# Performance work log

Measured on AMD Instinct MI355X. Metric: run time of the kernel, lower is better.

Reference implementation:

```python
import jax, jax.numpy as jnp
import numpy as np

L, N, C = 128, 32, 128
DIM_MLP, OUT = 128, 128


def setup_inputs() -> dict:
    key = jax.random.key(0)
    ks = jax.random.split(key, 6)
    s_in2 = 1.0 / np.sqrt(2 * C)
    s_mid = 1.0 / np.sqrt(DIM_MLP)
    s_in = 1.0 / np.sqrt(C)
    return {
        "x": jax.random.normal(ks[0], (L, N, C), jnp.float32),
        "attn_w1": jax.random.normal(ks[1], (2 * C, DIM_MLP), jnp.float32) * s_in2,
        "attn_b1": jnp.zeros((DIM_MLP,), jnp.float32),
        "attn_w2": jax.random.normal(ks[2], (DIM_MLP, OUT), jnp.float32) * s_mid,
        "attn_b2": jnp.zeros((OUT,), jnp.float32),
        "value_w1": jax.random.normal(ks[3], (C, DIM_MLP), jnp.float32) * s_in,
        "value_b1": jnp.zeros((DIM_MLP,), jnp.float32),
        "value_w2": jax.random.normal(ks[4], (DIM_MLP, OUT), jnp.float32) * s_mid,
        "value_b2": jnp.zeros((OUT,), jnp.float32),
    }


def reference(x, attn_w1, attn_b1, attn_w2, attn_b2,
              value_w1, value_b1, value_w2, value_b2):
    l, n, c = x.shape
    # Outer concat: pair[i, j, b] = concat(x[i, b], x[j, b])  -> (l, l, N, 2C)
    xi = jnp.broadcast_to(x[:, None, :, :], (l, l, n, c))
    xj = jnp.broadcast_to(x[None, :, :, :], (l, l, n, c))
    pair = jnp.concatenate([xi, xj], axis=-1)
    # Pairwise attention MLP (ReLU hidden, linear output)
    h = jax.nn.relu(pair @ attn_w1 + attn_b1)          # (l, l, N, dim_mlp)
    attn = h @ attn_w2 + attn_b2                       # (l, l, N, out)
    # Value MLP
    hv = jax.nn.relu(x @ value_w1 + value_b1)          # (l, N, dim_mlp)
    value = hv @ value_w2 + value_b2                   # (l, N, out)
    # Elementwise weighted reduce over key axis j (NOT a matmul over channels)
    out = jnp.einsum('ijbc,jbc->ibc', attn, value)     # (l, N, out)
    return out
```

## Files before the change

kernel.cpp:

```cpp
#include <hip/hip_runtime.h>
#include <hip/hip_bf16.h>

#define L_DIM 128
#define N_DIM 32
#define C_DIM 128
#define K_DIM 128
#define OUT_DIM 128

typedef __attribute__((ext_vector_type(8))) short short8;
typedef __attribute__((ext_vector_type(4))) float float4v;
typedef __attribute__((ext_vector_type(2))) float float2v;

static __device__ __forceinline__ short bf16_bits(float f) {
    __bf16 h = (__bf16)f;
    return __builtin_bit_cast(short, h);
}

__global__ __launch_bounds__(256) void k_pre(
    const float* __restrict__ x,
    const float* __restrict__ attn_w1, const float* __restrict__ attn_b1,
    const float* __restrict__ attn_w2,
    const float* __restrict__ value_w1, const float* __restrict__ value_b1,
    const float* __restrict__ value_w2, const float* __restrict__ value_b2,
    float* __restrict__ P, float* __restrict__ Q, float* __restrict__ V,
    short* __restrict__ W2s)
{
    int bid = blockIdx.x;
    if (bid >= 1024) {
        int e = (bid - 1024) * 256 + threadIdx.x;
        int idx  = e & 7;
        int colr = (e >> 3) & 15;
        int quad = (e >> 7) & 3;
        int mi   = (e >> 9) & 3;
        int ct   = e >> 11;
        int k = quad * 8 + 32 * mi + idx;
        int c = ct * 16 + colr;
        W2s[e] = bf16_bits(attn_w2[k * OUT_DIM + c]);
        return;
    }

    __shared__ float xs[4][C_DIM];
    __shared__ float hvs[4][K_DIM];
    int tid = threadIdx.x;
    int r0  = bid * 4;

    {
        int f = tid * 2;
        int row = f >> 7, c = f & 127;
        *(float2v*)(&xs[row][c]) = *(const float2v*)(x + (r0 + row) * C_DIM + c);
    }
    __syncthreads();

    int ks   = tid & 127;
    int half = tid >> 7;

    float pacc[2] = {0,0}, qacc[2] = {0,0}, hacc[2] = {0,0};
    #pragma unroll 4
    for (int c = 0; c < C_DIM; ++c) {
        float wa = attn_w1[c * K_DIM + ks];
        float wb = attn_w1[(C_DIM + c) * K_DIM + ks];
        float wv = value_w1[c * K_DIM + ks];
        #pragma unroll
        for (int r = 0; r < 2; ++r) {
            float xr = xs[half * 2 + r][c];
            pacc[r] = fmaf(xr, wa, pacc[r]);
            qacc[r] = fmaf(xr, wb, qacc[r]);
            hacc[r] = fmaf(xr, wv, hacc[r]);
        }
    }
    float b1 = attn_b1[ks], vb1 = value_b1[ks];
    #pragma unroll
    for (int r = 0; r < 2; ++r) {
        int rr = r0 + half * 2 + r;
        int i = rr >> 5, b = rr & 31;
        P[(b * L_DIM + i) * K_DIM + ks] = pacc[r];
        Q[(b * L_DIM + i) * K_DIM + ks] = qacc[r] + b1;
        hvs[half * 2 + r][ks] = fmaxf(hacc[r] + vb1, 0.f);
    }
    __syncthreads();

    float vacc[2] = {0,0};
    #pragma unroll 4
    for (int k = 0; k < K_DIM; ++k) {
        float w = value_w2[k * OUT_DIM + ks];
        #pragma unroll
        for (int r = 0; r < 2; ++r)
            vacc[r] = fmaf(hvs[half * 2 + r][k], w, vacc[r]);
    }
    float vb2 = value_b2[ks];
    #pragma unroll
    for (int r = 0; r < 2; ++r) {
        int rr = r0 + half * 2 + r;
        int i = rr >> 5, b = rr & 31;
        V[(b * L_DIM + i) * OUT_DIM + ks] = vacc[r] + vb2;
    }
}

__global__ __launch_bounds__(256) void k_sv(const float* __restrict__ V,
                                            float* __restrict__ Sv)
{
    __shared__ float red[256];
    int b = blockIdx.x;
    int tid = threadIdx.x;
    int c = tid & 127, jh = tid >> 7;
    float s = 0.f;
    #pragma unroll 4
    for (int jj = 0; jj < 64; ++jj)
        s += V[(b * L_DIM + jh * 64 + jj) * OUT_DIM + c];
    red[tid] = s;
    __syncthreads();
    if (tid < 128)
        Sv[b * OUT_DIM + tid] = red[tid] + red[128 + tid];
}

#define QV_STRIDE 132

__global__ __launch_bounds__(256)
__attribute__((amdgpu_waves_per_eu(2, 2)))
void k_main(
    const float* __restrict__ P, const float* __restrict__ Q,
    const float* __restrict__ V, const float* __restrict__ Sv,
    const short* __restrict__ W2s, const float* __restrict__ attn_b2,
    float* __restrict__ out)
{
    __shared__ short A_lds[4 * 256 * 8];
    __shared__ float QV_lds[2][2][16 * QV_STRIDE];
    __shared__ float P_lds[4 * K_DIM];

    int b     = blockIdx.x >> 5;
    int itile = blockIdx.x & 31;
    int tid   = threadIdx.x;
    int wave  = tid >> 6;
    int lane  = tid & 63;
    int quad  = lane >> 4;
    int col   = lane & 15;
    int i_g   = itile * 4 + wave;

    short8 bfrag[8][4];
    const short8* w2p = (const short8*)W2s;
    #pragma unroll
    for (int ct = 0; ct < 8; ++ct)
        #pragma unroll
        for (int mi = 0; mi < 4; ++mi)
            bfrag[ct][mi] = w2p[((ct * 4 + mi) * 4 + quad) * 16 + col];

    {
        int f = tid * 2;
        int ii = f >> 7, k = f & 127;
        *(float2v*)&P_lds[f] =
            *(const float2v*)(P + (b * L_DIM + itile * 4 + ii) * K_DIM + k);
    }

    int srow = tid >> 4;
    int sc8  = (tid & 15) * 8;
    const float* Qbase = Q + (size_t)(b * L_DIM) * K_DIM;
    const float* Vbase = V + (size_t)(b * L_DIM) * OUT_DIM;

    {
        const float* qp = Qbase + (0 * 16 + srow) * K_DIM + sc8;
        const float* vp = Vbase + (0 * 16 + srow) * OUT_DIM + sc8;
        float4v qa = *(const float4v*)qp, qb = *(const float4v*)(qp + 4);
        float4v va = *(const float4v*)vp, vb = *(const float4v*)(vp + 4);
        *(float4v*)&QV_lds[0][0][srow * QV_STRIDE + sc8]     = qa;
        *(float4v*)&QV_lds[0][0][srow * QV_STRIDE + sc8 + 4] = qb;
        *(float4v*)&QV_lds[0][1][srow * QV_STRIDE + sc8]     = va;
        *(float4v*)&QV_lds[0][1][srow * QV_STRIDE + sc8 + 4] = vb;
    }
    __syncthreads();

    float acc[8] = {0,0,0,0,0,0,0,0};
    int cur = 0;

    int m_  = tid >> 4;
    int kq_ = tid & 15;

    for (int r = 0; r < 8; ++r) {
        {
            const float* Qc = &QV_lds[cur][0][m_ * QV_STRIDE + kq_ * 8];
            float4v qa = *(const float4v*)Qc;
            float4v qb = *(const float4v*)(Qc + 4);
            #pragma unroll
            for (int i = 0; i < 4; ++i) {
                float4v pa = *(const float4v*)&P_lds[i * K_DIM + kq_ * 8];
                float4v pb = *(const float4v*)&P_lds[i * K_DIM + kq_ * 8 + 4];
                short8 a;
                #pragma unroll
                for (int t = 0; t < 4; ++t) {
                    a[t]     = bf16_bits(fmaxf(pa[t] + qa[t], 0.f));
                    a[t + 4] = bf16_bits(fmaxf(pb[t] + qb[t], 0.f));
                }
                *(short8*)&A_lds[(i * 256 + kq_ * 16 + (m_ ^ kq_)) * 8] = a;
            }
        }

        float4v nqa, nqb, nva, nvb;
        if (r < 7) {
            const float* qp = Qbase + ((r + 1) * 16 + srow) * K_DIM + sc8;
            const float* vp = Vbase + ((r + 1) * 16 + srow) * OUT_DIM + sc8;
            nqa = *(const float4v*)qp; nqb = *(const float4v*)(qp + 4);
            nva = *(const float4v*)vp; nvb = *(const float4v*)(vp + 4);
        }

        __syncthreads();

        int nxt = cur ^ 1;
        if (r < 7) {
            *(float4v*)&QV_lds[nxt][0][srow * QV_STRIDE + sc8]     = nqa;
            *(float4v*)&QV_lds[nxt][0][srow * QV_STRIDE + sc8 + 4] = nqb;
            *(float4v*)&QV_lds[nxt][1][srow * QV_STRIDE + sc8]     = nva;
            *(float4v*)&QV_lds[nxt][1][srow * QV_STRIDE + sc8 + 4] = nvb;
        }

        short8 af[4];
        #pragma unroll
        for (int ks = 0; ks < 4; ++ks) {
            int kq = ks * 4 + quad;
            af[ks] = *(const short8*)
                &A_lds[(wave * 256 + kq * 16 + (col ^ kq)) * 8];
        }
        const float* Vc = &QV_lds[cur][1][0];
        #pragma unroll
        for (int ct = 0; ct < 8; ++ct) {
            float4v c4 = {0.f, 0.f, 0.f, 0.f};
            #pragma unroll
            for (int ks = 0; ks < 4; ++ks)
                c4 = __builtin_amdgcn_mfma_f32_16x16x32_bf16(
                        af[ks], bfrag[ct][ks], c4, 0, 0, 0);
            int cc = ct * 16 + col;
            #pragma unroll
            for (int rr = 0; rr < 4; ++rr)
                acc[ct] = fmaf(c4[rr], Vc[(quad * 4 + rr) * QV_STRIDE + cc],
                               acc[ct]);
        }

        __syncthreads();
        cur ^= 1;
    }

    #pragma unroll
    for (int ct = 0; ct < 8; ++ct) {
        acc[ct] += __shfl_xor(acc[ct], 16, 64);
        acc[ct] += __shfl_xor(acc[ct], 32, 64);
    }

    if (quad == 0) {
        #pragma unroll
        for (int ct = 0; ct < 8; ++ct) {
            int cc = ct * 16 + col;
            out[(i_g * N_DIM + b) * OUT_DIM + cc] =
                acc[ct] + attn_b2[cc] * Sv[b * OUT_DIM + cc];
        }
    }
}

extern "C" void kernel_launch(void* const* d_in, const int* in_sizes, int n_in,
                              void* d_out, int out_size, void* d_ws, size_t ws_size,
                              hipStream_t stream)
{
    const float* x        = (const float*)d_in[0];
    const float* attn_w1  = (const float*)d_in[1];
    const float* attn_b1  = (const float*)d_in[2];
    const float* attn_w2  = (const float*)d_in[3];
    const float* attn_b2  = (const float*)d_in[4];
    const float* value_w1 = (const float*)d_in[5];
    const float* value_b1 = (const float*)d_in[6];
    const float* value_w2 = (const float*)d_in[7];
    const float* value_b2 = (const float*)d_in[8];
    float* out = (float*)d_out;

    float* ws  = (float*)d_ws;
    float* P   = ws;
    float* Q   = ws + 524288;
    float* V   = ws + 1048576;
    float* Sv  = ws + 1572864;
    short* W2s = (short*)(ws + 1576960);

    k_pre<<<1088, 256, 0, stream>>>(x, attn_w1, attn_b1, attn_w2,
                                    value_w1, value_b1, value_w2, value_b2,
                                    P, Q, V, W2s);
    k_sv<<<32, 256, 0, stream>>>(V, Sv);
    k_main<<<1024, 256, 0, stream>>>(P, Q, V, Sv, W2s, attn_b2, out);
}
```

Measured before the change: 127.6 us.

## Build MFMA A-fragments in registers, double i-rows per block, fold value-sum into main

The main kernel now builds the ReLU(P+Q) bf16 A fragments directly in registers instead of staging them through LDS, which removes one barrier per iteration. Each wave processes two query rows, so every loaded Q/V tile and the preloaded W2 fragments are reused twice and the grid halves. The separate column-sum kernel is dropped; the sum of V over the key axis is accumulated inside the main loop. The pre kernel handles 16 rows per block to reuse weight loads. The trade-off is higher register pressure and fewer blocks, which lowers occupancy.

```diff
diff --git a/kernel.cpp b/kernel.cpp
--- a/kernel.cpp
+++ b/kernel.cpp
@@ -7,9 +7,10 @@
 #define K_DIM 128
 #define OUT_DIM 128
 
+#define QV_STRIDE 132
+
 typedef __attribute__((ext_vector_type(8))) short short8;
 typedef __attribute__((ext_vector_type(4))) float float4v;
-typedef __attribute__((ext_vector_type(2))) float float2v;
 
 static __device__ __forceinline__ short bf16_bits(float f) {
     __bf16 h = (__bf16)f;
@@ -26,8 +27,8 @@
     short* __restrict__ W2s)
 {
     int bid = blockIdx.x;
-    if (bid >= 1024) {
-        int e = (bid - 1024) * 256 + threadIdx.x;
+    if (bid >= 256) {
+        int e = (bid - 256) * 256 + threadIdx.x;
         int idx  = e & 7;
         int colr = (e >> 3) & 15;
         int quad = (e >> 7) & 3;
@@ -39,30 +40,33 @@
         return;
     }
 
-    __shared__ float xs[4][C_DIM];
-    __shared__ float hvs[4][K_DIM];
+    __shared__ float xs[16][C_DIM];
+    __shared__ float hvs[16][K_DIM];
     int tid = threadIdx.x;
-    int r0  = bid * 4;
+    int r0  = bid * 16;
 
     {
-        int f = tid * 2;
+        int f = tid * 8;
         int row = f >> 7, c = f & 127;
-        *(float2v*)(&xs[row][c]) = *(const float2v*)(x + (r0 + row) * C_DIM + c);
+        *(float4v*)(&xs[row][c])     = *(const float4v*)(x + (r0 + row) * C_DIM + c);
+        *(float4v*)(&xs[row][c + 4]) = *(const float4v*)(x + (r0 + row) * C_DIM + c + 4);
     }
     __syncthreads();
 
     int ks   = tid & 127;
     int half = tid >> 7;
 
-    float pacc[2] = {0,0}, qacc[2] = {0,0}, hacc[2] = {0,0};
+    float pacc[8] = {0,0,0,0,0,0,0,0};
+    float qacc[8] = {0,0,0,0,0,0,0,0};
+    float hacc[8] = {0,0,0,0,0,0,0,0};
     #pragma unroll 4
     for (int c = 0; c < C_DIM; ++c) {
         float wa = attn_w1[c * K_DIM + ks];
         float wb = attn_w1[(C_DIM + c) * K_DIM + ks];
         float wv = value_w1[c * K_DIM + ks];
         #pragma unroll
-        for (int r = 0; r < 2; ++r) {
-            float xr = xs[half * 2 + r][c];
+        for (int r = 0; r < 8; ++r) {
+            float xr = xs[half * 8 + r][c];
             pacc[r] = fmaf(xr, wa, pacc[r]);
             qacc[r] = fmaf(xr, wb, qacc[r]);
             hacc[r] = fmaf(xr, wv, hacc[r]);
@@ -70,71 +74,51 @@
     }
     float b1 = attn_b1[ks], vb1 = value_b1[ks];
     #pragma unroll
-    for (int r = 0; r < 2; ++r) {
-        int rr = r0 + half * 2 + r;
-        int i = rr >> 5, b = rr & 31;
-        P[(b * L_DIM + i) * K_DIM + ks] = pacc[r];
-        Q[(b * L_DIM + i) * K_DIM + ks] = qacc[r] + b1;
-        hvs[half * 2 + r][ks] = fmaxf(hacc[r] + vb1, 0.f);
+    for (int r = 0; r < 8; ++r) {
+        int rr = r0 + half * 8 + r;
+        int i = rr >> 5, bb = rr & 31;
+        P[(bb * L_DIM + i) * K_DIM + ks] = pacc[r];
+        Q[(bb * L_DIM + i) * K_DIM + ks] = qacc[r] + b1;
+        hvs[half * 8 + r][ks] = fmaxf(hacc[r] + vb1, 0.f);
     }
     __syncthreads();
 
-    float vacc[2] = {0,0};
+    float vacc[8] = {0,0,0,0,0,0,0,0};
     #pragma unroll 4
     for (int k = 0; k < K_DIM; ++k) {
         float w = value_w2[k * OUT_DIM + ks];
         #pragma unroll
-        for (int r = 0; r < 2; ++r)
-            vacc[r] = fmaf(hvs[half * 2 + r][k], w, vacc[r]);
+        for (int r = 0; r < 8; ++r)
+            vacc[r] = fmaf(hvs[half * 8 + r][k], w, vacc[r]);
     }
     float vb2 = value_b2[ks];
     #pragma unroll
-    for (int r = 0; r < 2; ++r) {
-        int rr = r0 + half * 2 + r;
-        int i = rr >> 5, b = rr & 31;
-        V[(b * L_DIM + i) * OUT_DIM + ks] = vacc[r] + vb2;
-    }
-}
-
-__global__ __launch_bounds__(256) void k_sv(const float* __restrict__ V,
-                                            float* __restrict__ Sv)
-{
-    __shared__ float red[256];
-    int b = blockIdx.x;
-    int tid = threadIdx.x;
-    int c = tid & 127, jh = tid >> 7;
-    float s = 0.f;
-    #pragma unroll 4
-    for (int jj = 0; jj < 64; ++jj)
-        s += V[(b * L_DIM + jh * 64 + jj) * OUT_DIM + c];
-    red[tid] = s;
-    __syncthreads();
-    if (tid < 128)
-        Sv[b * OUT_DIM + tid] = red[tid] + red[128 + tid];
-}
-
-#define QV_STRIDE 132
+    for (int r = 0; r < 8; ++r) {
+        int rr = r0 + half * 8 + r;
+        int i = rr >> 5, bb = rr & 31;
+        V[(bb * L_DIM + i) * OUT_DIM + ks] = vacc[r] + vb2;
+    }
+}
 
 __global__ __launch_bounds__(256)
 __attribute__((amdgpu_waves_per_eu(2, 2)))
 void k_main(
     const float* __restrict__ P, const float* __restrict__ Q,
-    const float* __restrict__ V, const float* __restrict__ Sv,
+    const float* __restrict__ V,
     const short* __restrict__ W2s, const float* __restrict__ attn_b2,
     float* __restrict__ out)
 {
-    __shared__ short A_lds[4 * 256 * 8];
-    __shared__ float QV_lds[2][2][16 * QV_STRIDE];
-    __shared__ float P_lds[4 * K_DIM];
-
-    int b     = blockIdx.x >> 5;
-    int itile = blockIdx.x & 31;
+    __shared__ float Q_lds[2][16 * QV_STRIDE];
+    __shared__ float V_lds[2][16 * QV_STRIDE];
+    __shared__ float P_lds[8 * K_DIM];
+
+    int b     = blockIdx.x >> 4;
+    int itile = blockIdx.x & 15;
     int tid   = threadIdx.x;
     int wave  = tid >> 6;
     int lane  = tid & 63;
     int quad  = lane >> 4;
     int col   = lane & 15;
-    int i_g   = itile * 4 + wave;
 
     short8 bfrag[8][4];
     const short8* w2p = (const short8*)W2s;
@@ -145,10 +129,10 @@
             bfrag[ct][mi] = w2p[((ct * 4 + mi) * 4 + quad) * 16 + col];
 
     {
-        int f = tid * 2;
+        int f = tid * 4;
         int ii = f >> 7, k = f & 127;
-        *(float2v*)&P_lds[f] =
-            *(const float2v*)(P + (b * L_DIM + itile * 4 + ii) * K_DIM + k);
+        *(float4v*)&P_lds[f] =
+            *(const float4v*)(P + (b * L_DIM + itile * 8 + ii) * K_DIM + k);
     }
 
     int srow = tid >> 4;
@@ -157,39 +141,44 @@
     const float* Vbase = V + (size_t)(b * L_DIM) * OUT_DIM;
 
     {
-        const float* qp = Qbase + (0 * 16 + srow) * K_DIM + sc8;
-        const float* vp = Vbase + (0 * 16 + srow) * OUT_DIM + sc8;
+        const float* qp = Qbase + srow * K_DIM + sc8;
+        const float* vp = Vbase + srow * OUT_DIM + sc8;
         float4v qa = *(const float4v*)qp, qb = *(const float4v*)(qp + 4);
         float4v va = *(const float4v*)vp, vb = *(const float4v*)(vp + 4);
-        *(float4v*)&QV_lds[0][0][srow * QV_STRIDE + sc8]     = qa;
-        *(float4v*)&QV_lds[0][0][srow * QV_STRIDE + sc8 + 4] = qb;
-        *(float4v*)&QV_lds[0][1][srow * QV_STRIDE + sc8]     = va;
-        *(float4v*)&QV_lds[0][1][srow * QV_STRIDE + sc8 + 4] = vb;
+        *(float4v*)&Q_lds[0][srow * QV_STRIDE + sc8]     = qa;
+        *(float4v*)&Q_lds[0][srow * QV_STRIDE + sc8 + 4] = qb;
+        *(float4v*)&V_lds[0][srow * QV_STRIDE + sc8]     = va;
+        *(float4v*)&V_lds[0][srow * QV_STRIDE + sc8 + 4] = vb;
     }
     __syncthreads();
 
-    float acc[8] = {0,0,0,0,0,0,0,0};
-    int cur = 0;
-
-    int m_  = tid >> 4;
-    int kq_ = tid & 15;
+    float acc[2][8] = {};
+    float sv[8]     = {};
 
     for (int r = 0; r < 8; ++r) {
-        {
-            const float* Qc = &QV_lds[cur][0][m_ * QV_STRIDE + kq_ * 8];
-            float4v qa = *(const float4v*)Qc;
-            float4v qb = *(const float4v*)(Qc + 4);
+        int cur = r & 1;
+
+        short8 af[2][4];
+        const float* Qc = &Q_lds[cur][col * QV_STRIDE + quad * 8];
+        #pragma unroll
+        for (int ksl = 0; ksl < 4; ++ksl) {
+            float4v q0 = *(const float4v*)(Qc + ksl * 32);
+            float4v q1 = *(const float4v*)(Qc + ksl * 32 + 4);
             #pragma unroll
-            for (int i = 0; i < 4; ++i) {
-                float4v pa = *(const float4v*)&P_lds[i * K_DIM + kq_ * 8];
-                float4v pb = *(const float4v*)&P_lds[i * K_DIM + kq_ * 8 + 4];
+            for (int ii = 0; ii < 2; ++ii) {
+                const float* Pc =
+                    &P_lds[(wave * 2 + ii) * K_DIM + ksl * 32 + quad * 8];
+                float4v pa = *(const float4v*)Pc;
+                float4v pb = *(const float4v*)(Pc + 4);
+                float4v sa = pa + q0;
+                float4v sb = pb + q1;
                 short8 a;
                 #pragma unroll
                 for (int t = 0; t < 4; ++t) {
-                    a[t]     = bf16_bits(fmaxf(pa[t] + qa[t], 0.f));
-                    a[t + 4] = bf16_bits(fmaxf(pb[t] + qb[t], 0.f));
+                    a[t]     = bf16_bits(fmaxf(sa[t], 0.f));
+                    a[t + 4] = bf16_bits(fmaxf(sb[t], 0.f));
                 }
-                *(short8*)&A_lds[(i * 256 + kq_ * 16 + (m_ ^ kq_)) * 8] = a;
+                af[ii][ksl] = a;
             }
         }
 
@@ -201,54 +190,56 @@
             nva = *(const float4v*)vp; nvb = *(const float4v*)(vp + 4);
         }
 
-        __syncthreads();
-
-        int nxt = cur ^ 1;
-        if (r < 7) {
-            *(float4v*)&QV_lds[nxt][0][srow * QV_STRIDE + sc8]     = nqa;
-            *(float4v*)&QV_lds[nxt][0][srow * QV_STRIDE + sc8 + 4] = nqb;
-            *(float4v*)&QV_lds[nxt][1][srow * QV_STRIDE + sc8]     = nva;
-            *(float4v*)&QV_lds[nxt][1][srow * QV_STRIDE + sc8 + 4] = nvb;
-        }
-
-        short8 af[4];
-        #pragma unroll
-        for (int ks = 0; ks < 4; ++ks) {
-            int kq = ks * 4 + quad;
-            af[ks] = *(const short8*)
-                &A_lds[(wave * 256 + kq * 16 + (col ^ kq)) * 8];
-        }
-        const float* Vc = &QV_lds[cur][1][0];
+        const float* Vc = &V_lds[cur][0];
         #pragma unroll
         for (int ct = 0; ct < 8; ++ct) {
-            float4v c4 = {0.f, 0.f, 0.f, 0.f};
+            float4v c0 = {0.f, 0.f, 0.f, 0.f};
+            float4v c1 = {0.f, 0.f, 0.f, 0.f};
             #pragma unroll
-            for (int ks = 0; ks < 4; ++ks)
-                c4 = __builtin_amdgcn_mfma_f32_16x16x32_bf16(
-                        af[ks], bfrag[ct][ks], c4, 0, 0, 0);
+            for (int ksl = 0; ksl < 4; ++ksl) {
+                c0 = __builtin_amdgcn_mfma_f32_16x16x32_bf16(
+                        af[0][ksl], bfrag[ct][ksl], c0, 0, 0, 0);
+                c1 = __builtin_amdgcn_mfma_f32_16x16x32_bf16(
+                        af[1][ksl], bfrag[ct][ksl], c1, 0, 0, 0);
+            }
             int cc = ct * 16 + col;
             #pragma unroll
-            for (int rr = 0; rr < 4; ++rr)
-                acc[ct] = fmaf(c4[rr], Vc[(quad * 4 + rr) * QV_STRIDE + cc],
-                               acc[ct]);
-        }
-
-        __syncthreads();
-        cur ^= 1;
+            for (int rr = 0; rr < 4; ++rr) {
+                float v = Vc[(quad * 4 + rr) * QV_STRIDE + cc];
+                acc[0][ct] = fmaf(c0[rr], v, acc[0][ct]);
+                acc[1][ct] = fmaf(c1[rr], v, acc[1][ct]);
+                sv[ct] += v;
+            }
+        }
+
+        if (r < 7) {
+            int nxt = cur ^ 1;
+            *(float4v*)&Q_lds[nxt][srow * QV_STRIDE + sc8]     = nqa;
+            *(float4v*)&Q_lds[nxt][srow * QV_STRIDE + sc8 + 4] = nqb;
+            *(float4v*)&V_lds[nxt][srow * QV_STRIDE + sc8]     = nva;
+            *(float4v*)&V_lds[nxt][srow * QV_STRIDE + sc8 + 4] = nvb;
+            __syncthreads();
+        }
     }
 
     #pragma unroll
     for (int ct = 0; ct < 8; ++ct) {
-        acc[ct] += __shfl_xor(acc[ct], 16, 64);
-        acc[ct] += __shfl_xor(acc[ct], 32, 64);
-    }
-
-    if (quad == 0) {
-        #pragma unroll
-        for (int ct = 0; ct < 8; ++ct) {
+        acc[0][ct] += __shfl_xor(acc[0][ct], 16, 64);
+        acc[0][ct] += __shfl_xor(acc[0][ct], 32, 64);
+        acc[1][ct] += __shfl_xor(acc[1][ct], 16, 64);
+        acc[1][ct] += __shfl_xor(acc[1][ct], 32, 64);
+        sv[ct]     += __shfl_xor(sv[ct], 16, 64);
+        sv[ct]     += __shfl_xor(sv[ct], 32, 64);
+    }
+
+    int ig = itile * 8 + wave * 2 + (quad >> 1);
+    #pragma unroll
+    for (int ct = 0; ct < 8; ++ct) {
+        float a = (quad < 2) ? acc[0][ct] : acc[1][ct];
+        if ((quad & 1) == (ct >> 2)) {
             int cc = ct * 16 + col;
-            out[(i_g * N_DIM + b) * OUT_DIM + cc] =
-                acc[ct] + attn_b2[cc] * Sv[b * OUT_DIM + cc];
+            out[(ig * N_DIM + b) * OUT_DIM + cc] =
+                a + attn_b2[cc] * sv[ct];
         }
     }
 }
@@ -272,12 +263,10 @@
     float* P   = ws;
     float* Q   = ws + 524288;
     float* V   = ws + 1048576;
-    float* Sv  = ws + 1572864;
-    short* W2s = (short*)(ws + 1576960);
-
-    k_pre<<<1088, 256, 0, stream>>>(x, attn_w1, attn_b1, attn_w2,
-                                    value_w1, value_b1, value_w2, value_b2,
-                                    P, Q, V, W2s);
-    k_sv<<<32, 256, 0, stream>>>(V, Sv);
-    k_main<<<1024, 256, 0, stream>>>(P, Q, V, Sv, W2s, attn_b2, out);
-}
+    short* W2s = (short*)(ws + 1572864);
+
+    k_pre<<<320, 256, 0, stream>>>(x, attn_w1, attn_b1, attn_w2,
+                                   value_w1, value_b1, value_w2, value_b2,
+                                   P, Q, V, W2s);
+    k_main<<<512, 256, 0, stream>>>(P, Q, V, W2s, attn_b2, out);
+}
```

New measurement: 147.6 us. +15.7%, slower.
